# Optimization experiments

Measured on AMD Instinct MI355X. Metric: run time of the kernel, lower is better.

The kernel has to match this reference:

```python
import jax, jax.numpy as jnp
import numpy as np

B, N, D = 512, 128, 128
VALID = 64                      # valid atoms per molecule (structured mask)
N_NODES = B * VALID             # 32768
DEG = 16
N_EDGES = N_NODES * DEG         # 524288
L = 3                           # predictor_layer_num
NUM_TASKS = 12
ATOM_VOCAB, EDGE_VOCAB = 119, 8


def _ln(x, g, b, eps=1e-5):
    mu = jnp.mean(x, -1, keepdims=True)
    v = jnp.mean((x - mu) ** 2, -1, keepdims=True)
    return (x - mu) * jax.lax.rsqrt(v + eps) * g + b


def _gelu(x):
    return jax.nn.gelu(x, approximate=False)  # torch F.gelu default (erf)


def setup_inputs():
    key = jax.random.key(0)
    ks = jax.random.split(key, 40)
    s = 0.02
    d = {}
    d['logits'] = jax.random.normal(ks[0], (B, N, D), jnp.float32)
    d['atom_mask'] = jnp.broadcast_to(jnp.arange(N) < VALID, (B, N))
    d['atom_feature'] = jax.random.randint(ks[1], (N_NODES,), 0, ATOM_VOCAB)
    d['edge_index'] = jax.random.randint(ks[2], (2, N_EDGES), 0, N_NODES)
    d['edge_attr'] = jax.random.randint(ks[3], (N_EDGES,), 0, EDGE_VOCAB)
    d['batch_idx'] = jnp.arange(N_NODES) // VALID
    # GNN encoder params
    d['atom_emb'] = s * jax.random.normal(ks[4], (ATOM_VOCAB, D))
    d['edge_emb'] = s * jax.random.normal(ks[5], (EDGE_VOCAB, D))
    d['gnn_W1'] = s * jax.random.normal(ks[6], (L, D, 2 * D))
    d['gnn_b1'] = jnp.zeros((L, 2 * D))
    d['gnn_W2'] = s * jax.random.normal(ks[7], (L, 2 * D, D))
    d['gnn_b2'] = jnp.zeros((L, D))
    d['gnn_ln_g'] = jnp.ones((L, D))
    d['gnn_ln_b'] = jnp.zeros((L, D))
    # attention pooling gate_nn: Linear(d,2d)->LN->ReLU->Linear(2d,1)
    d['gate_W1'] = s * jax.random.normal(ks[8], (D, 2 * D))
    d['gate_b1'] = jnp.zeros((2 * D,))
    d['gate_ln_g'] = jnp.ones((2 * D,))
    d['gate_ln_b'] = jnp.zeros((2 * D,))
    d['gate_W2'] = s * jax.random.normal(ks[9], (2 * D, 1))
    d['gate_b2'] = jnp.zeros((1,))
    # 2 residual blocks
    d['res_fc1_W'] = s * jax.random.normal(ks[10], (2, D, D))
    d['res_fc1_b'] = jnp.zeros((2, D))
    d['res_ln1_g'] = jnp.ones((2, D))
    d['res_ln1_b'] = jnp.zeros((2, D))
    d['res_fc2_W'] = s * jax.random.normal(ks[11], (2, D, D))
    d['res_fc2_b'] = jnp.zeros((2, D))
    d['res_ln2_g'] = jnp.ones((2, D))
    d['res_ln2_b'] = jnp.zeros((2, D))
    # prediction head
    d['pred_W1'] = s * jax.random.normal(ks[12], (D, D))
    d['pred_b1'] = jnp.zeros((D,))
    d['pred_W2'] = s * jax.random.normal(ks[13], (D, NUM_TASKS))
    d['pred_b2'] = jnp.zeros((NUM_TASKS,))
    return d


def reference(logits, atom_mask, atom_feature, edge_index, edge_attr, batch_idx,
              atom_emb, edge_emb, gnn_W1, gnn_b1, gnn_W2, gnn_b2, gnn_ln_g, gnn_ln_b,
              gate_W1, gate_b1, gate_ln_g, gate_ln_b, gate_W2, gate_b2,
              res_fc1_W, res_fc1_b, res_ln1_g, res_ln1_b,
              res_fc2_W, res_fc2_b, res_ln2_g, res_ln2_b,
              pred_W1, pred_b1, pred_W2, pred_b2):
    # boolean-mask gather: flat_atom_feat[flat_mask] with static masked count
    flat_mask = atom_mask.reshape(-1)
    idx = jnp.nonzero(flat_mask, size=N_NODES)[0]
    x = logits.reshape(-1, D)[idx]                       # [N_NODES, D]
    x = x + atom_emb[atom_feature]                       # incorporate atom features
    src, dst = edge_index[0], edge_index[1]
    e_emb = edge_emb[edge_attr]                          # [E, D]
    # residual GIN-style message passing, JK='last', eval (no dropout)
    for l in range(L):
        msg = jax.nn.relu(x[src] + e_emb)                # [E, D] irregular gather
        agg = jax.ops.segment_sum(msg, dst, num_segments=N_NODES)
        h = jax.nn.relu(agg @ gnn_W1[l] + gnn_b1[l]) @ gnn_W2[l] + gnn_b2[l]
        x = x + _ln(h, gnn_ln_g[l], gnn_ln_b[l])
    # attentional aggregation: segment softmax over nodes per graph
    gate = jax.nn.relu(_ln(x @ gate_W1 + gate_b1, gate_ln_g, gate_ln_b)) @ gate_W2 + gate_b2  # [n,1]
    gm = jax.ops.segment_max(gate, batch_idx, num_segments=B)
    e = jnp.exp(gate - gm[batch_idx])
    den = jax.ops.segment_sum(e, batch_idx, num_segments=B)
    w = e / den[batch_idx]
    g = jax.ops.segment_sum(w * x, batch_idx, num_segments=B)  # [B, D]
    # 2 residual MLP blocks (eval: dropout = identity)
    for r in range(2):
        h = _gelu(_ln(g @ res_fc1_W[r] + res_fc1_b[r], res_ln1_g[r], res_ln1_b[r]))
        h = _ln(h @ res_fc2_W[r] + res_fc2_b[r], res_ln2_g[r], res_ln2_b[r])
        g = g + h
    # prediction head
    return _gelu(g @ pred_W1 + pred_b1) @ pred_W2 + pred_b2  # [B, NUM_TASKS]
```

## Files before the change

### kernel.cpp

```cpp
#include <hip/hip_runtime.h>
#include <hip/hip_bf16.h>

#define N_NODES 32768
#define N_EDGES 524288
#define B_GRAPHS 512

typedef __attribute__((ext_vector_type(8))) short sh8;
typedef __attribute__((ext_vector_type(4))) float f32x4;

__device__ __forceinline__ unsigned short f2b(float f) {
    unsigned int u = __float_as_uint(f);
    return (unsigned short)((u + 0x7FFFu + ((u >> 16) & 1u)) >> 16);
}
__device__ __forceinline__ float blo(unsigned int u) { return __uint_as_float(u << 16); }
__device__ __forceinline__ float bhi(unsigned int u) { return __uint_as_float(u & 0xFFFF0000u); }
__device__ __forceinline__ float gelu_exact(float z) {
    return 0.5f * z * (1.0f + erff(z * 0.70710678118654752440f));
}

#define PREP_BLOCKS 896
#define BX_BLOCKS 4096

__global__ __launch_bounds__(256) void k_prep(const float* __restrict__ W1,
                                              const float* __restrict__ W2,
                                              const float* __restrict__ gW1,
                                              const float* __restrict__ logits,
                                              const int* __restrict__ feat,
                                              const float* __restrict__ aemb,
                                              unsigned short* __restrict__ W1T,
                                              unsigned short* __restrict__ W2T,
                                              unsigned short* __restrict__ gW1T,
                                              int* __restrict__ deg,
                                              float* __restrict__ x,
                                              unsigned short* __restrict__ xb) {
    int bb = blockIdx.x;
    if (bb < PREP_BLOCKS) {
        int tid = bb * 256 + threadIdx.x;
        if (tid < N_NODES) deg[tid] = 0;
        int m = tid >> 15, i = tid & 32767;
        if (m < 3) {
            int r = i >> 8, c = i & 255;
            W1T[m * 32768 + c * 128 + r] = f2b(W1[m * 32768 + i]);
        } else if (m < 6) {
            int mm = m - 3;
            int r = i >> 7, c = i & 127;
            W2T[mm * 32768 + c * 256 + r] = f2b(W2[mm * 32768 + i]);
        } else {
            int r = i >> 8, c = i & 255;
            gW1T[c * 128 + r] = f2b(gW1[i]);
        }
    } else {
        int idx = (bb - PREP_BLOCKS) * 256 + threadIdx.x;
        int n = idx >> 5, c = idx & 31;
        int srow = ((n >> 6) << 7) + (n & 63);
        float4 lv = ((const float4*)logits)[srow * 32 + c];
        float4 av = ((const float4*)aemb)[feat[n] * 32 + c];
        float4 o;
        o.x = lv.x + av.x; o.y = lv.y + av.y; o.z = lv.z + av.z; o.w = lv.w + av.w;
        ((float4*)x)[idx] = o;
        ushort4 ob;
        ob.x = f2b(o.x); ob.y = f2b(o.y); ob.z = f2b(o.z); ob.w = f2b(o.w);
        ((ushort4*)xb)[idx] = ob;
    }
}

__global__ void k_deg(const int* __restrict__ dst, int* __restrict__ deg) {
    int e = blockIdx.x * blockDim.x + threadIdx.x;
    if (e < N_EDGES) atomicAdd(&deg[dst[e]], 1);
}

__global__ __launch_bounds__(1024) void k_scan(const int* __restrict__ deg,
                                               int* __restrict__ offs,
                                               int* __restrict__ cursor) {
    int tid = threadIdx.x;
    int lane = tid & 63, wid = tid >> 6;
    int base = tid * 32;
    int pref[32];
    int run = 0;
    #pragma unroll
    for (int i = 0; i < 32; i++) { pref[i] = run; run += deg[base + i]; }
    int s = run;
    for (int m = 1; m < 64; m <<= 1) { int t = __shfl_up(s, m); if (lane >= m) s += t; }
    __shared__ int wsum[16];
    if (lane == 63) wsum[wid] = s;
    __syncthreads();
    if (tid < 16) {
        int v = wsum[tid];
        for (int m = 1; m < 16; m <<= 1) { int t = __shfl_up(v, m, 16); if (tid >= m) v += t; }
        wsum[tid] = v;
    }
    __syncthreads();
    int wbase = wid ? wsum[wid - 1] : 0;
    int ebase = wbase + (s - run);
    #pragma unroll
    for (int i = 0; i < 32; i++) {
        int o = ebase + pref[i];
        offs[base + i] = o;
        cursor[base + i] = o;
    }
    if (tid == 1023) offs[N_NODES] = ebase + run;
}

__global__ void k_scatter(const int* __restrict__ src, const int* __restrict__ dst,
                          const int* __restrict__ attr, int* __restrict__ cursor,
                          int* __restrict__ csr) {
    int e = blockIdx.x * blockDim.x + threadIdx.x;
    if (e < N_EDGES) {
        int p = atomicAdd(&cursor[dst[e]], 1);
        csr[p] = src[e] | (attr[e] << 16);
    }
}

__global__ __launch_bounds__(256) void k_agg(const unsigned short* __restrict__ xb,
                                             const int* __restrict__ offs,
                                             const int* __restrict__ csr,
                                             const float* __restrict__ eemb,
                                             unsigned short* __restrict__ aggb,
                                             int half) {
    __shared__ float semb[8 * 64];
    int tid = threadIdx.x;
    int fbase = half * 64;
    for (int i = tid; i < 512; i += 256)
        semb[i] = eemb[(i >> 6) * 128 + fbase + (i & 63)];
    __syncthreads();
    int node = blockIdx.x * 4 + (tid >> 6);
    int lane = tid & 63;
    int li = lane & 31, h = lane >> 5;
    int o0 = offs[node], o1 = offs[node + 1];
    int deg = o1 - o0;
    int degc = deg < 64 ? deg : 64;
    int ed = (lane < degc) ? csr[o0 + lane] : 0;
    float a0 = 0.f, a1 = 0.f;
    int nh0 = (degc + 1) >> 1;
    int nhl = h ? (degc >> 1) : nh0;
    int j = 0;
    for (; j + 8 <= nh0; j += 8) {
        int pk[8]; unsigned int u[8];
        #pragma unroll
        for (int t = 0; t < 8; t++) pk[t] = __shfl(ed, h + 2 * (j + t));
        #pragma unroll
        for (int t = 0; t < 8; t++)
            u[t] = *(const unsigned int*)(xb + (size_t)(pk[t] & 0xFFFF) * 128 + fbase + li * 2);
        #pragma unroll
        for (int t = 0; t < 8; t++) {
            if (j + t < nhl) {
                float2 ev = *(const float2*)&semb[(pk[t] >> 16) * 64 + li * 2];
                a0 += fmaxf(blo(u[t]) + ev.x, 0.f);
                a1 += fmaxf(bhi(u[t]) + ev.y, 0.f);
            }
        }
    }
    for (; j < nh0; j++) {
        int pk = __shfl(ed, h + 2 * j);
        unsigned int u = *(const unsigned int*)(xb + (size_t)(pk & 0xFFFF) * 128 + fbase + li * 2);
        if (j < nhl) {
            float2 ev = *(const float2*)&semb[(pk >> 16) * 64 + li * 2];
            a0 += fmaxf(blo(u) + ev.x, 0.f);
            a1 += fmaxf(bhi(u) + ev.y, 0.f);
        }
    }
    for (int i = 64 + h; i < deg; i += 2) {
        int pk = csr[o0 + i];
        unsigned int u = *(const unsigned int*)(xb + (size_t)(pk & 0xFFFF) * 128 + fbase + li * 2);
        float2 ev = *(const float2*)&semb[(pk >> 16) * 64 + li * 2];
        a0 += fmaxf(blo(u) + ev.x, 0.f);
        a1 += fmaxf(bhi(u) + ev.y, 0.f);
    }
    a0 += __shfl_xor(a0, 32);
    a1 += __shfl_xor(a1, 32);
    if (h == 0) {
        unsigned int wv = (unsigned int)f2b(a0) | ((unsigned int)f2b(a1) << 16);
        *(unsigned int*)(aggb + (size_t)node * 128 + fbase + li * 2) = wv;
    }
}

__global__ __launch_bounds__(512) void k_layer(const unsigned short* __restrict__ A,
                                               const unsigned short* __restrict__ W1T,
                                               const float* __restrict__ b1,
                                               const unsigned short* __restrict__ W2T,
                                               const float* __restrict__ b2,
                                               const float* __restrict__ lng,
                                               const float* __restrict__ lnb,
                                               float* __restrict__ x,
                                               unsigned short* __restrict__ xb) {
    __shared__ __align__(16) unsigned short WS[33792];
    __shared__ __align__(16) unsigned short T[128][264];
    int tid = threadIdx.x;
    int row0 = blockIdx.x * 128;
    int l = tid & 63, w = tid >> 6;
    int fr = l & 15, hi = l >> 4, fk = hi * 8;
    sh8 afr[4];
    #pragma unroll
    for (int kc = 0; kc < 4; kc++)
        afr[kc] = *(const sh8*)(A + (size_t)(row0 + w * 16 + fr) * 128 + kc * 32 + fk);
    #pragma unroll
    for (int s = tid; s < 4096; s += 512) {
        int n = s >> 4, k8 = s & 15;
        *(uint4*)&WS[n * 132 + k8 * 8] = *(const uint4*)(W1T + (size_t)n * 128 + k8 * 8);
    }
    __syncthreads();
    #pragma unroll
    for (int ch = 0; ch < 2; ch++) {
        f32x4 acc[8];
        #pragma unroll
        for (int c = 0; c < 8; c++) acc[c] = (f32x4){0.f, 0.f, 0.f, 0.f};
        #pragma unroll
        for (int kc = 0; kc < 4; kc++) {
            #pragma unroll
            for (int c = 0; c < 8; c++) {
                sh8 b = *(const sh8*)&WS[(ch * 128 + c * 16 + fr) * 132 + kc * 32 + fk];
                acc[c] = __builtin_amdgcn_mfma_f32_16x16x32_bf16(afr[kc], b, acc[c], 0, 0, 0);
            }
        }
        int rb = w * 16 + hi * 4;
        #pragma unroll
        for (int c = 0; c < 8; c++) {
            int col = ch * 128 + c * 16 + fr;
            float bv = b1[col];
            #pragma unroll
            for (int q = 0; q < 4; q++)
                T[rb + q][col] = f2b(fmaxf(acc[c][q] + bv, 0.f));
        }
    }
    __syncthreads();
    #pragma unroll
    for (int s = tid; s < 4096; s += 512) {
        int n = s >> 5, k8 = s & 31;
        *(uint4*)&WS[n * 264 + k8 * 8] = *(const uint4*)(W2T + (size_t)n * 256 + k8 * 8);
    }
    __syncthreads();
    f32x4 acc[8];
    #pragma unroll
    for (int c = 0; c < 8; c++) acc[c] = (f32x4){0.f, 0.f, 0.f, 0.f};
    #pragma unroll 2
    for (int kc = 0; kc < 8; kc++) {
        sh8 a = *(const sh8*)&T[w * 16 + fr][kc * 32 + fk];
        #pragma unroll
        for (int c = 0; c < 8; c++) {
            sh8 b = *(const sh8*)&WS[(c * 16 + fr) * 264 + kc * 32 + fk];
            acc[c] = __builtin_amdgcn_mfma_f32_16x16x32_bf16(a, b, acc[c], 0, 0, 0);
        }
    }
    float s0 = 0.f, s1 = 0.f, s2 = 0.f, s3 = 0.f;
    float q0 = 0.f, q1 = 0.f, q2 = 0.f, q3 = 0.f;
    #pragma unroll
    for (int c = 0; c < 8; c++) {
        float bv = b2[c * 16 + fr];
        #pragma unroll
        for (int q = 0; q < 4; q++) acc[c][q] += bv;
        s0 += acc[c][0]; q0 += acc[c][0] * acc[c][0];
        s1 += acc[c][1]; q1 += acc[c][1] * acc[c][1];
        s2 += acc[c][2]; q2 += acc[c][2] * acc[c][2];
        s3 += acc[c][3]; q3 += acc[c][3] * acc[c][3];
    }
    #pragma unroll
    for (int m = 1; m < 16; m <<= 1) {
        s0 += __shfl_xor(s0, m); q0 += __shfl_xor(q0, m);
        s1 += __shfl_xor(s1, m); q1 += __shfl_xor(q1, m);
        s2 += __shfl_xor(s2, m); q2 += __shfl_xor(q2, m);
        s3 += __shfl_xor(s3, m); q3 += __shfl_xor(q3, m);
    }
    float mu[4], rs_[4];
    mu[0] = s0 * (1.f / 128.f); rs_[0] = rsqrtf(q0 * (1.f / 128.f) - mu[0] * mu[0] + 1e-5f);
    mu[1] = s1 * (1.f / 128.f); rs_[1] = rsqrtf(q1 * (1.f / 128.f) - mu[1] * mu[1] + 1e-5f);
    mu[2] = s2 * (1.f / 128.f); rs_[2] = rsqrtf(q2 * (1.f / 128.f) - mu[2] * mu[2] + 1e-5f);
    mu[3] = s3 * (1.f / 128.f); rs_[3] = rsqrtf(q3 * (1.f / 128.f) - mu[3] * mu[3] + 1e-5f);
    int rbase = row0 + w * 16 + hi * 4;
    #pragma unroll
    for (int c = 0; c < 8; c++) {
        int col = c * 16 + fr;
        float g = lng[col], bb = lnb[col];
        #pragma unroll
        for (int q = 0; q < 4; q++) {
            size_t idx = (size_t)(rbase + q) * 128 + col;
            float nx = x[idx] + (acc[c][q] - mu[q]) * rs_[q] * g + bb;
            x[idx] = nx;
            xb[idx] = f2b(nx);
        }
    }
}

__global__ __launch_bounds__(512) void k_gpt(const unsigned short* __restrict__ xbin,
        const float* __restrict__ xf,
        const unsigned short* __restrict__ gW1T,
        const float* __restrict__ b1,
        const float* __restrict__ lng, const float* __restrict__ lnb,
        const float* __restrict__ w2, const float* __restrict__ b2,
        const float* __restrict__ fc1W, const float* __restrict__ fc1b,
        const float* __restrict__ ln1g, const float* __restrict__ ln1b,
        const float* __restrict__ fc2W, const float* __restrict__ fc2b,
        const float* __restrict__ ln2g, const float* __restrict__ ln2b,
        const float* __restrict__ pW1, const float* __restrict__ pb1,
        const float* __restrict__ pW2, const float* __restrict__ pb2,
        float* __restrict__ out) {
    __shared__ __align__(16) unsigned short WS[33792];
    __shared__ __align__(16) unsigned short T[128][264];
    __shared__ float gates[128];
    __shared__ float pooled[2][128];
    __shared__ float shh[2][128];
    __shared__ float ps[2][2], pq[2][2];
    int tid = threadIdx.x;
    int row0 = blockIdx.x * 128;
    int l = tid & 63, w = tid >> 6;
    int fr = l & 15, hi = l >> 4, fk = hi * 8;
    sh8 afr[4];
    #pragma unroll
    for (int kc = 0; kc < 4; kc++)
        afr[kc] = *(const sh8*)(xbin + (size_t)(row0 + w * 16 + fr) * 128 + kc * 32 + fk);
    #pragma unroll
    for (int s = tid; s < 4096; s += 512) {
        int n = s >> 4, k8 = s & 15;
        *(uint4*)&WS[n * 132 + k8 * 8] = *(const uint4*)(gW1T + (size_t)n * 128 + k8 * 8);
    }
    __syncthreads();
    #pragma unroll
    for (int ch = 0; ch < 2; ch++) {
        f32x4 acc[8];
        #pragma unroll
        for (int c = 0; c < 8; c++) acc[c] = (f32x4){0.f, 0.f, 0.f, 0.f};
        #pragma unroll
        for (int kc = 0; kc < 4; kc++) {
            #pragma unroll
            for (int c = 0; c < 8; c++) {
                sh8 b = *(const sh8*)&WS[(ch * 128 + c * 16 + fr) * 132 + kc * 32 + fk];
                acc[c] = __builtin_amdgcn_mfma_f32_16x16x32_bf16(afr[kc], b, acc[c], 0, 0, 0);
            }
        }
        int rb = w * 16 + hi * 4;
        #pragma unroll
        for (int c = 0; c < 8; c++) {
            int col = ch * 128 + c * 16 + fr;
            float bv = b1[col];
            #pragma unroll
            for (int q = 0; q < 4; q++)
                T[rb + q][col] = f2b(acc[c][q] + bv);
        }
    }
    __syncthreads();
    {
        int row = tid >> 2, qd = tid & 3;
        float s = 0.f, sq = 0.f;
        #pragma unroll 4
        for (int j = 0; j < 16; j++) {
            uint2 u = *(const uint2*)&T[row][qd * 64 + j * 4];
            float v0 = blo(u.x), v1 = bhi(u.x), v2 = blo(u.y), v3 = bhi(u.y);
            s += v0 + v1 + v2 + v3;
            sq += v0 * v0 + v1 * v1 + v2 * v2 + v3 * v3;
        }
        s += __shfl_xor(s, 1); s += __shfl_xor(s, 2);
        sq += __shfl_xor(sq, 1); sq += __shfl_xor(sq, 2);
        float mu = s * (1.f / 256.f);
        float rcp = rsqrtf(sq * (1.f / 256.f) - mu * mu + 1e-5f);
        float acc = 0.f;
        #pragma unroll 4
        for (int j = 0; j < 16; j++) {
            int col = qd * 64 + j * 4;
            uint2 u = *(const uint2*)&T[row][col];
            float4 g4 = *(const float4*)&lng[col];
            float4 e4 = *(const float4*)&lnb[col];
            float4 w4 = *(const float4*)&w2[col];
            acc += fmaxf((blo(u.x) - mu) * rcp * g4.x + e4.x, 0.f) * w4.x;
            acc += fmaxf((bhi(u.x) - mu) * rcp * g4.y + e4.y, 0.f) * w4.y;
            acc += fmaxf((blo(u.y) - mu) * rcp * g4.z + e4.z, 0.f) * w4.z;
            acc += fmaxf((bhi(u.y) - mu) * rcp * g4.w + e4.w, 0.f) * w4.w;
        }
        acc += __shfl_xor(acc, 1); acc += __shfl_xor(acc, 2);
        if (qd == 0) gates[row] = acc + b2[0];
    }
    __syncthreads();
    int g = tid >> 8, t2 = tid & 255;
    if (t2 < 64) {
        float gv = gates[g * 64 + t2];
        float m = gv;
        #pragma unroll
        for (int mk = 1; mk < 64; mk <<= 1) m = fmaxf(m, __shfl_xor(m, mk));
        float e = expf(gv - m);
        float s = e;
        #pragma unroll
        for (int mk = 1; mk < 64; mk <<= 1) s += __shfl_xor(s, mk);
        gates[g * 64 + t2] = e / s;
    }
    __syncthreads();
    int d = t2 & 127, hh = t2 >> 7;
    float pacc = 0.f;
    for (int i = hh * 32; i < hh * 32 + 32; i++)
        pacc += gates[g * 64 + i] * xf[(size_t)(row0 + g * 64 + i) * 128 + d];
    if (hh == 0) pooled[g][d] = pacc;
    __syncthreads();
    if (hh == 1) pooled[g][d] += pacc;
    __syncthreads();
    int wv = t2 >> 6;
    for (int r = 0; r < 2; r++) {
        float acc = 0.f, s = 0.f, q = 0.f;
        if (t2 < 128) {
            const float* W1 = fc1W + r * 16384;
            acc = fc1b[r * 128 + t2];
            for (int k = 0; k < 128; k++) acc += pooled[g][k] * W1[k * 128 + t2];
            s = acc; q = acc * acc;
            #pragma unroll
            for (int m = 1; m < 64; m <<= 1) { s += __shfl_xor(s, m); q += __shfl_xor(q, m); }
            if ((t2 & 63) == 0) { ps[g][wv] = s; pq[g][wv] = q; }
        }
        __syncthreads();
        if (t2 < 128) {
            float S = ps[g][0] + ps[g][1], Q = pq[g][0] + pq[g][1];
            float mu = S * (1.f / 128.f);
            float var = Q * (1.f / 128.f) - mu * mu;
            float z = (acc - mu) * rsqrtf(var + 1e-5f) * ln1g[r * 128 + t2] + ln1b[r * 128 + t2];
            shh[g][t2] = gelu_exact(z);
        }
        __syncthreads();
        float acc2 = 0.f;
        if (t2 < 128) {
            const float* W2 = fc2W + r * 16384;
            acc2 = fc2b[r * 128 + t2];
            for (int k = 0; k < 128; k++) acc2 += shh[g][k] * W2[k * 128 + t2];
            s = acc2; q = acc2 * acc2;
            #pragma unroll
            for (int m = 1; m < 64; m <<= 1) { s += __shfl_xor(s, m); q += __shfl_xor(q, m); }
            if ((t2 & 63) == 0) { ps[g][wv] = s; pq[g][wv] = q; }
        }
        __syncthreads();
        if (t2 < 128) {
            float S = ps[g][0] + ps[g][1], Q = pq[g][0] + pq[g][1];
            float mu = S * (1.f / 128.f);
            float var = Q * (1.f / 128.f) - mu * mu;
            float z2 = (acc2 - mu) * rsqrtf(var + 1e-5f) * ln2g[r * 128 + t2] + ln2b[r * 128 + t2];
            pooled[g][t2] = pooled[g][t2] + z2;
        }
        __syncthreads();
    }
    float hacc = 0.f;
    if (t2 < 128) {
        hacc = pb1[t2];
        for (int k = 0; k < 128; k++) hacc += pooled[g][k] * pW1[k * 128 + t2];
    }
    __syncthreads();
    if (t2 < 128) shh[g][t2] = gelu_exact(hacc);
    __syncthreads();
    if (t2 < 12) {
        float o = pb2[t2];
        for (int k = 0; k < 128; k++) o += shh[g][k] * pW2[k * 12 + t2];
        out[(size_t)(blockIdx.x * 2 + g) * 12 + t2] = o;
    }
}

extern "C" void kernel_launch(void* const* d_in, const int* in_sizes, int n_in,
                              void* d_out, int out_size, void* d_ws, size_t ws_size,
                              hipStream_t stream) {
    const float* logits    = (const float*)d_in[0];
    const int*   atom_feat = (const int*)d_in[2];
    const int*   edge_src  = (const int*)d_in[3];
    const int*   edge_dst  = edge_src + N_EDGES;
    const int*   edge_attr = (const int*)d_in[4];
    const float* atom_emb  = (const float*)d_in[6];
    const float* edge_emb  = (const float*)d_in[7];
    const float* gnn_W1    = (const float*)d_in[8];
    const float* gnn_b1    = (const float*)d_in[9];
    const float* gnn_W2    = (const float*)d_in[10];
    const float* gnn_b2    = (const float*)d_in[11];
    const float* gnn_ln_g  = (const float*)d_in[12];
    const float* gnn_ln_b  = (const float*)d_in[13];
    const float* gate_W1   = (const float*)d_in[14];
    const float* gate_b1   = (const float*)d_in[15];
    const float* gate_ln_g = (const float*)d_in[16];
    const float* gate_ln_b = (const float*)d_in[17];
    const float* gate_W2   = (const float*)d_in[18];
    const float* gate_b2   = (const float*)d_in[19];
    const float* res_fc1_W = (const float*)d_in[20];
    const float* res_fc1_b = (const float*)d_in[21];
    const float* res_ln1_g = (const float*)d_in[22];
    const float* res_ln1_b = (const float*)d_in[23];
    const float* res_fc2_W = (const float*)d_in[24];
    const float* res_fc2_b = (const float*)d_in[25];
    const float* res_ln2_g = (const float*)d_in[26];
    const float* res_ln2_b = (const float*)d_in[27];
    const float* pred_W1   = (const float*)d_in[28];
    const float* pred_b1   = (const float*)d_in[29];
    const float* pred_W2   = (const float*)d_in[30];
    const float* pred_b2   = (const float*)d_in[31];
    float* out = (float*)d_out;

    char* w = (char*)d_ws;
    float*          x    = (float*)w;          w += (size_t)N_NODES * 128 * 4;
    unsigned short* xb   = (unsigned short*)w; w += (size_t)N_NODES * 128 * 2;
    unsigned short* aggb = (unsigned short*)w; w += (size_t)N_NODES * 128 * 2;
    unsigned short* W1T  = (unsigned short*)w; w += 3 * 32768 * 2;
    unsigned short* W2T  = (unsigned short*)w; w += 3 * 32768 * 2;
    unsigned short* gW1T = (unsigned short*)w; w += 32768 * 2;
    int*   deg    = (int*)w;   w += N_NODES * 4;
    int*   offs   = (int*)w;   w += (N_NODES + 64) * 4;
    int*   cursor = (int*)w;   w += N_NODES * 4;
    int*   csr    = (int*)w;   w += N_EDGES * 4;

    k_prep<<<PREP_BLOCKS + BX_BLOCKS, 256, 0, stream>>>(
        gnn_W1, gnn_W2, gate_W1, logits, atom_feat, atom_emb,
        W1T, W2T, gW1T, deg, x, xb);
    k_deg<<<N_EDGES / 256, 256, 0, stream>>>(edge_dst, deg);
    k_scan<<<1, 1024, 0, stream>>>(deg, offs, cursor);
    k_scatter<<<N_EDGES / 256, 256, 0, stream>>>(edge_src, edge_dst, edge_attr, cursor, csr);

    for (int l = 0; l < 3; l++) {
        k_agg<<<N_NODES / 4, 256, 0, stream>>>(xb, offs, csr, edge_emb, aggb, 0);
        k_agg<<<N_NODES / 4, 256, 0, stream>>>(xb, offs, csr, edge_emb, aggb, 1);
        k_layer<<<N_NODES / 128, 512, 0, stream>>>(
            aggb, W1T + l * 32768, gnn_b1 + l * 256,
            W2T + l * 32768, gnn_b2 + l * 128,
            gnn_ln_g + l * 128, gnn_ln_b + l * 128, x, xb);
    }

    k_gpt<<<N_NODES / 128, 512, 0, stream>>>(
        xb, x, gW1T, gate_b1, gate_ln_g, gate_ln_b, gate_W2, gate_b2,
        res_fc1_W, res_fc1_b, res_ln1_g, res_ln1_b,
        res_fc2_W, res_fc2_b, res_ln2_g, res_ln2_b,
        pred_W1, pred_b1, pred_W2, pred_b2, out);
}
```

Measured before the change: 303.4 us.

## Split fused gate/pool/tail kernel into three kernels with register-resident gate LN

Replaces the single fused gate+pool+MLP-tail kernel with three kernels. The gate kernel now keeps the 256-wide MFMA accumulators in registers and does the LayerNorm and dot product with cross-lane shuffles, so the bf16 staging tile in shared memory goes away. Pooling and the residual/prediction MLP tail move to per-graph kernels with 512 blocks each, giving more parallelism in the latency-bound tail. The cost is two extra launches and a round trip of gate values and pooled vectors through global memory.

```diff
diff --git a/kernel.cpp b/kernel.cpp
--- a/kernel.cpp
+++ b/kernel.cpp
@@ -280,12 +280,127 @@
     }
 }
 
-__global__ __launch_bounds__(512) void k_gpt(const unsigned short* __restrict__ xbin,
-        const float* __restrict__ xf,
-        const unsigned short* __restrict__ gW1T,
-        const float* __restrict__ b1,
-        const float* __restrict__ lng, const float* __restrict__ lnb,
-        const float* __restrict__ w2, const float* __restrict__ b2,
+__global__ __launch_bounds__(512) void k_gate2(const unsigned short* __restrict__ xbin,
+                                               const unsigned short* __restrict__ gW1T,
+                                               const float* __restrict__ b1,
+                                               const float* __restrict__ lng,
+                                               const float* __restrict__ lnb,
+                                               const float* __restrict__ w2,
+                                               const float* __restrict__ b2,
+                                               float* __restrict__ gate) {
+    __shared__ __align__(16) unsigned short WS[33792];
+    int tid = threadIdx.x;
+    int row0 = blockIdx.x * 128;
+    int l = tid & 63, w = tid >> 6;
+    int fr = l & 15, hi = l >> 4, fk = hi * 8;
+    sh8 afr[4];
+    #pragma unroll
+    for (int kc = 0; kc < 4; kc++)
+        afr[kc] = *(const sh8*)(xbin + (size_t)(row0 + w * 16 + fr) * 128 + kc * 32 + fk);
+    #pragma unroll
+    for (int s = tid; s < 4096; s += 512) {
+        int n = s >> 4, k8 = s & 15;
+        *(uint4*)&WS[n * 132 + k8 * 8] = *(const uint4*)(gW1T + (size_t)n * 128 + k8 * 8);
+    }
+    __syncthreads();
+    f32x4 acc[2][8];
+    #pragma unroll
+    for (int ch = 0; ch < 2; ch++)
+        #pragma unroll
+        for (int c = 0; c < 8; c++) acc[ch][c] = (f32x4){0.f, 0.f, 0.f, 0.f};
+    #pragma unroll
+    for (int kc = 0; kc < 4; kc++) {
+        #pragma unroll
+        for (int ch = 0; ch < 2; ch++) {
+            #pragma unroll
+            for (int c = 0; c < 8; c++) {
+                sh8 b = *(const sh8*)&WS[(ch * 128 + c * 16 + fr) * 132 + kc * 32 + fk];
+                acc[ch][c] = __builtin_amdgcn_mfma_f32_16x16x32_bf16(afr[kc], b, acc[ch][c], 0, 0, 0);
+            }
+        }
+    }
+    float s[4] = {0.f, 0.f, 0.f, 0.f}, q[4] = {0.f, 0.f, 0.f, 0.f};
+    #pragma unroll
+    for (int ch = 0; ch < 2; ch++) {
+        #pragma unroll
+        for (int c = 0; c < 8; c++) {
+            float bv = b1[ch * 128 + c * 16 + fr];
+            #pragma unroll
+            for (int qd = 0; qd < 4; qd++) {
+                float v = acc[ch][c][qd] + bv;
+                acc[ch][c][qd] = v;
+                s[qd] += v; q[qd] += v * v;
+            }
+        }
+    }
+    #pragma unroll
+    for (int m = 1; m < 16; m <<= 1) {
+        #pragma unroll
+        for (int qd = 0; qd < 4; qd++) {
+            s[qd] += __shfl_xor(s[qd], m);
+            q[qd] += __shfl_xor(q[qd], m);
+        }
+    }
+    float mu[4], rcp[4];
+    #pragma unroll
+    for (int qd = 0; qd < 4; qd++) {
+        mu[qd] = s[qd] * (1.f / 256.f);
+        rcp[qd] = rsqrtf(q[qd] * (1.f / 256.f) - mu[qd] * mu[qd] + 1e-5f);
+    }
+    float dot[4] = {0.f, 0.f, 0.f, 0.f};
+    #pragma unroll
+    for (int ch = 0; ch < 2; ch++) {
+        #pragma unroll
+        for (int c = 0; c < 8; c++) {
+            int col = ch * 128 + c * 16 + fr;
+            float g = lng[col], bb = lnb[col], ww = w2[col];
+            #pragma unroll
+            for (int qd = 0; qd < 4; qd++) {
+                float z = (acc[ch][c][qd] - mu[qd]) * rcp[qd] * g + bb;
+                dot[qd] += fmaxf(z, 0.f) * ww;
+            }
+        }
+    }
+    #pragma unroll
+    for (int m = 1; m < 16; m <<= 1)
+        #pragma unroll
+        for (int qd = 0; qd < 4; qd++) dot[qd] += __shfl_xor(dot[qd], m);
+    if (fr == 0) {
+        float b2v = b2[0];
+        #pragma unroll
+        for (int qd = 0; qd < 4; qd++)
+            gate[row0 + w * 16 + hi * 4 + qd] = dot[qd] + b2v;
+    }
+}
+
+__global__ __launch_bounds__(256) void k_pool(const float* __restrict__ x,
+                                              const float* __restrict__ gate,
+                                              float* __restrict__ g) {
+    __shared__ float sw[64];
+    __shared__ float sacc[128];
+    int b = blockIdx.x, tid = threadIdx.x;
+    if (tid < 64) {
+        float gv = gate[b * 64 + tid];
+        float m = gv;
+        #pragma unroll
+        for (int mk = 1; mk < 64; mk <<= 1) m = fmaxf(m, __shfl_xor(m, mk));
+        float e = expf(gv - m);
+        float s = e;
+        #pragma unroll
+        for (int mk = 1; mk < 64; mk <<= 1) s += __shfl_xor(s, mk);
+        sw[tid] = e / s;
+    }
+    __syncthreads();
+    int d = tid & 127, h = tid >> 7;
+    float acc = 0.f;
+    for (int i = h * 32; i < h * 32 + 32; i++)
+        acc += sw[i] * x[(size_t)(b * 64 + i) * 128 + d];
+    if (h == 0) sacc[d] = acc;
+    __syncthreads();
+    if (h == 1) g[b * 128 + d] = sacc[d] + acc;
+}
+
+__global__ __launch_bounds__(128) void k_tail(const float* __restrict__ g_in,
         const float* __restrict__ fc1W, const float* __restrict__ fc1b,
         const float* __restrict__ ln1g, const float* __restrict__ ln1b,
         const float* __restrict__ fc2W, const float* __restrict__ fc2b,
@@ -293,155 +408,56 @@
         const float* __restrict__ pW1, const float* __restrict__ pb1,
         const float* __restrict__ pW2, const float* __restrict__ pb2,
         float* __restrict__ out) {
-    __shared__ __align__(16) unsigned short WS[33792];
-    __shared__ __align__(16) unsigned short T[128][264];
-    __shared__ float gates[128];
-    __shared__ float pooled[2][128];
-    __shared__ float shh[2][128];
-    __shared__ float ps[2][2], pq[2][2];
-    int tid = threadIdx.x;
-    int row0 = blockIdx.x * 128;
-    int l = tid & 63, w = tid >> 6;
-    int fr = l & 15, hi = l >> 4, fk = hi * 8;
-    sh8 afr[4];
-    #pragma unroll
-    for (int kc = 0; kc < 4; kc++)
-        afr[kc] = *(const sh8*)(xbin + (size_t)(row0 + w * 16 + fr) * 128 + kc * 32 + fk);
-    #pragma unroll
-    for (int s = tid; s < 4096; s += 512) {
-        int n = s >> 4, k8 = s & 15;
-        *(uint4*)&WS[n * 132 + k8 * 8] = *(const uint4*)(gW1T + (size_t)n * 128 + k8 * 8);
-    }
-    __syncthreads();
-    #pragma unroll
-    for (int ch = 0; ch < 2; ch++) {
-        f32x4 acc[8];
-        #pragma unroll
-        for (int c = 0; c < 8; c++) acc[c] = (f32x4){0.f, 0.f, 0.f, 0.f};
-        #pragma unroll
-        for (int kc = 0; kc < 4; kc++) {
-            #pragma unroll
-            for (int c = 0; c < 8; c++) {
-                sh8 b = *(const sh8*)&WS[(ch * 128 + c * 16 + fr) * 132 + kc * 32 + fk];
-                acc[c] = __builtin_amdgcn_mfma_f32_16x16x32_bf16(afr[kc], b, acc[c], 0, 0, 0);
-            }
-        }
-        int rb = w * 16 + hi * 4;
-        #pragma unroll
-        for (int c = 0; c < 8; c++) {
-            int col = ch * 128 + c * 16 + fr;
-            float bv = b1[col];
-            #pragma unroll
-            for (int q = 0; q < 4; q++)
-                T[rb + q][col] = f2b(acc[c][q] + bv);
-        }
-    }
-    __syncthreads();
-    {
-        int row = tid >> 2, qd = tid & 3;
-        float s = 0.f, sq = 0.f;
-        #pragma unroll 4
-        for (int j = 0; j < 16; j++) {
-            uint2 u = *(const uint2*)&T[row][qd * 64 + j * 4];
-            float v0 = blo(u.x), v1 = bhi(u.x), v2 = blo(u.y), v3 = bhi(u.y);
-            s += v0 + v1 + v2 + v3;
-            sq += v0 * v0 + v1 * v1 + v2 * v2 + v3 * v3;
-        }
-        s += __shfl_xor(s, 1); s += __shfl_xor(s, 2);
-        sq += __shfl_xor(sq, 1); sq += __shfl_xor(sq, 2);
-        float mu = s * (1.f / 256.f);
-        float rcp = rsqrtf(sq * (1.f / 256.f) - mu * mu + 1e-5f);
-        float acc = 0.f;
-        #pragma unroll 4
-        for (int j = 0; j < 16; j++) {
-            int col = qd * 64 + j * 4;
-            uint2 u = *(const uint2*)&T[row][col];
-            float4 g4 = *(const float4*)&lng[col];
-            float4 e4 = *(const float4*)&lnb[col];
-            float4 w4 = *(const float4*)&w2[col];
-            acc += fmaxf((blo(u.x) - mu) * rcp * g4.x + e4.x, 0.f) * w4.x;
-            acc += fmaxf((bhi(u.x) - mu) * rcp * g4.y + e4.y, 0.f) * w4.y;
-            acc += fmaxf((blo(u.y) - mu) * rcp * g4.z + e4.z, 0.f) * w4.z;
-            acc += fmaxf((bhi(u.y) - mu) * rcp * g4.w + e4.w, 0.f) * w4.w;
-        }
-        acc += __shfl_xor(acc, 1); acc += __shfl_xor(acc, 2);
-        if (qd == 0) gates[row] = acc + b2[0];
-    }
-    __syncthreads();
-    int g = tid >> 8, t2 = tid & 255;
-    if (t2 < 64) {
-        float gv = gates[g * 64 + t2];
-        float m = gv;
-        #pragma unroll
-        for (int mk = 1; mk < 64; mk <<= 1) m = fmaxf(m, __shfl_xor(m, mk));
-        float e = expf(gv - m);
-        float s = e;
-        #pragma unroll
-        for (int mk = 1; mk < 64; mk <<= 1) s += __shfl_xor(s, mk);
-        gates[g * 64 + t2] = e / s;
-    }
-    __syncthreads();
-    int d = t2 & 127, hh = t2 >> 7;
-    float pacc = 0.f;
-    for (int i = hh * 32; i < hh * 32 + 32; i++)
-        pacc += gates[g * 64 + i] * xf[(size_t)(row0 + g * 64 + i) * 128 + d];
-    if (hh == 0) pooled[g][d] = pacc;
-    __syncthreads();
-    if (hh == 1) pooled[g][d] += pacc;
-    __syncthreads();
-    int wv = t2 >> 6;
+    __shared__ float sg[128], sh[128];
+    __shared__ float ps[2], pq[2];
+    int b = blockIdx.x, tid = threadIdx.x;
+    int w = tid >> 6;
+    sg[tid] = g_in[b * 128 + tid];
+    __syncthreads();
     for (int r = 0; r < 2; r++) {
-        float acc = 0.f, s = 0.f, q = 0.f;
-        if (t2 < 128) {
-            const float* W1 = fc1W + r * 16384;
-            acc = fc1b[r * 128 + t2];
-            for (int k = 0; k < 128; k++) acc += pooled[g][k] * W1[k * 128 + t2];
-            s = acc; q = acc * acc;
-            #pragma unroll
-            for (int m = 1; m < 64; m <<= 1) { s += __shfl_xor(s, m); q += __shfl_xor(q, m); }
-            if ((t2 & 63) == 0) { ps[g][wv] = s; pq[g][wv] = q; }
-        }
-        __syncthreads();
-        if (t2 < 128) {
-            float S = ps[g][0] + ps[g][1], Q = pq[g][0] + pq[g][1];
-            float mu = S * (1.f / 128.f);
-            float var = Q * (1.f / 128.f) - mu * mu;
-            float z = (acc - mu) * rsqrtf(var + 1e-5f) * ln1g[r * 128 + t2] + ln1b[r * 128 + t2];
-            shh[g][t2] = gelu_exact(z);
-        }
-        __syncthreads();
-        float acc2 = 0.f;
-        if (t2 < 128) {
-            const float* W2 = fc2W + r * 16384;
-            acc2 = fc2b[r * 128 + t2];
-            for (int k = 0; k < 128; k++) acc2 += shh[g][k] * W2[k * 128 + t2];
-            s = acc2; q = acc2 * acc2;
-            #pragma unroll
-            for (int m = 1; m < 64; m <<= 1) { s += __shfl_xor(s, m); q += __shfl_xor(q, m); }
-            if ((t2 & 63) == 0) { ps[g][wv] = s; pq[g][wv] = q; }
-        }
-        __syncthreads();
-        if (t2 < 128) {
-            float S = ps[g][0] + ps[g][1], Q = pq[g][0] + pq[g][1];
-            float mu = S * (1.f / 128.f);
-            float var = Q * (1.f / 128.f) - mu * mu;
-            float z2 = (acc2 - mu) * rsqrtf(var + 1e-5f) * ln2g[r * 128 + t2] + ln2b[r * 128 + t2];
-            pooled[g][t2] = pooled[g][t2] + z2;
-        }
-        __syncthreads();
-    }
-    float hacc = 0.f;
-    if (t2 < 128) {
-        hacc = pb1[t2];
-        for (int k = 0; k < 128; k++) hacc += pooled[g][k] * pW1[k * 128 + t2];
-    }
-    __syncthreads();
-    if (t2 < 128) shh[g][t2] = gelu_exact(hacc);
-    __syncthreads();
-    if (t2 < 12) {
-        float o = pb2[t2];
-        for (int k = 0; k < 128; k++) o += shh[g][k] * pW2[k * 12 + t2];
-        out[(size_t)(blockIdx.x * 2 + g) * 12 + t2] = o;
+        const float* W1 = fc1W + r * 16384;
+        float acc = fc1b[r * 128 + tid];
+        for (int k = 0; k < 128; k++) acc += sg[k] * W1[k * 128 + tid];
+        float s = acc, q = acc * acc;
+        #pragma unroll
+        for (int m = 1; m < 64; m <<= 1) { s += __shfl_xor(s, m); q += __shfl_xor(q, m); }
+        __syncthreads();
+        if ((tid & 63) == 0) { ps[w] = s; pq[w] = q; }
+        __syncthreads();
+        float S = ps[0] + ps[1], Q = pq[0] + pq[1];
+        float mu = S * (1.f / 128.f);
+        float var = Q * (1.f / 128.f) - mu * mu;
+        float z = (acc - mu) * rsqrtf(var + 1e-5f) * ln1g[r * 128 + tid] + ln1b[r * 128 + tid];
+        z = gelu_exact(z);
+        __syncthreads();
+        sh[tid] = z;
+        __syncthreads();
+        const float* W2 = fc2W + r * 16384;
+        float acc2 = fc2b[r * 128 + tid];
+        for (int k = 0; k < 128; k++) acc2 += sh[k] * W2[k * 128 + tid];
+        s = acc2; q = acc2 * acc2;
+        #pragma unroll
+        for (int m = 1; m < 64; m <<= 1) { s += __shfl_xor(s, m); q += __shfl_xor(q, m); }
+        __syncthreads();
+        if ((tid & 63) == 0) { ps[w] = s; pq[w] = q; }
+        __syncthreads();
+        S = ps[0] + ps[1]; Q = pq[0] + pq[1];
+        mu = S * (1.f / 128.f);
+        var = Q * (1.f / 128.f) - mu * mu;
+        float z2 = (acc2 - mu) * rsqrtf(var + 1e-5f) * ln2g[r * 128 + tid] + ln2b[r * 128 + tid];
+        __syncthreads();
+        sg[tid] = sg[tid] + z2;
+        __syncthreads();
+    }
+    float acc = pb1[tid];
+    for (int k = 0; k < 128; k++) acc += sg[k] * pW1[k * 128 + tid];
+    __syncthreads();
+    sh[tid] = gelu_exact(acc);
+    __syncthreads();
+    if (tid < 12) {
+        float o = pb2[tid];
+        for (int k = 0; k < 128; k++) o += sh[k] * pW2[k * 12 + tid];
+        out[b * 12 + tid] = o;
     }
 }
 
@@ -492,6 +508,8 @@
     int*   offs   = (int*)w;   w += (N_NODES + 64) * 4;
     int*   cursor = (int*)w;   w += N_NODES * 4;
     int*   csr    = (int*)w;   w += N_EDGES * 4;
+    float* gate   = (float*)w; w += N_NODES * 4;
+    float* gpool  = (float*)w; w += B_GRAPHS * 128 * 4;
 
     k_prep<<<PREP_BLOCKS + BX_BLOCKS, 256, 0, stream>>>(
         gnn_W1, gnn_W2, gate_W1, logits, atom_feat, atom_emb,
@@ -509,8 +527,10 @@
             gnn_ln_g + l * 128, gnn_ln_b + l * 128, x, xb);
     }
 
-    k_gpt<<<N_NODES / 128, 512, 0, stream>>>(
-        xb, x, gW1T, gate_b1, gate_ln_g, gate_ln_b, gate_W2, gate_b2,
+    k_gate2<<<N_NODES / 128, 512, 0, stream>>>(
+        xb, gW1T, gate_b1, gate_ln_g, gate_ln_b, gate_W2, gate_b2, gate);
+    k_pool<<<B_GRAPHS, 256, 0, stream>>>(x, gate, gpool);
+    k_tail<<<B_GRAPHS, 128, 0, stream>>>(gpool,
         res_fc1_W, res_fc1_b, res_ln1_g, res_ln1_b,
         res_fc2_W, res_fc2_b, res_ln2_g, res_ln2_b,
         pred_W1, pred_b1, pred_W2, pred_b2, out);
```

Result: no change. 301.7 us (-0.6%).
